# Kernel optimization log

Hardware: AMD Instinct MI355X
Metric: run time of the kernel (lower is better)

Reference implementation:

```python
import jax, jax.numpy as jnp
import numpy as np

H, W = 30, 30
D = 256
MAX_OBJECTS = 16
SENT = H * W  # sentinel label for background / invalid slots


def label_components(grid):
    """4-connected same-color connected-component labeling.
    grid: [B,H,W] int32. Returns labels [B,H,W] where each foreground cell
    carries the minimum linear index of its component (== raster-scan BFS
    discovery order of the torch code), SENT for background."""
    B = grid.shape[0]
    lin = jnp.arange(H * W, dtype=jnp.int32).reshape(1, H, W)
    fg = grid > 0
    init = jnp.where(fg, lin, SENT).astype(jnp.int32)
    big = jnp.int32(SENT)

    def nbr_min(lab):
        lp = jnp.pad(lab, ((0, 0), (1, 1), (1, 1)), constant_values=SENT)
        gp = jnp.pad(grid, ((0, 0), (1, 1), (1, 1)), constant_values=-1)
        m = lab
        for di, dj in ((-1, 0), (1, 0), (0, -1), (0, 1)):
            ls = lp[:, 1 + di:1 + di + H, 1 + dj:1 + dj + W]
            gs = gp[:, 1 + di:1 + di + H, 1 + dj:1 + dj + W]
            m = jnp.minimum(m, jnp.where(gs == grid, ls, big))
        return jnp.where(fg, m, big)

    def cond(s):
        return s[1]

    def body(s):
        lab, _ = s
        new = nbr_min(lab)
        # pointer jumping: label <- min(label, label[label]) accelerates convergence
        flat = new.reshape(B, H * W)
        jumped = jnp.take_along_axis(flat, jnp.clip(flat, 0, H * W - 1), axis=1)
        flat = jnp.where(flat < SENT, jnp.minimum(flat, jumped), SENT)
        new = flat.reshape(B, H, W)
        return new, jnp.any(new != lab)

    labels, _ = jax.lax.while_loop(cond, body, (init, jnp.array(True)))
    return labels


def extract_objects(grid, labels):
    """Per-slot (color, y, x, h, w, valid), each [B, MAX_OBJECTS]."""
    B = grid.shape[0]
    HW = H * W
    lin = jnp.arange(HW, dtype=jnp.int32)
    rows, cols = lin // W, lin % W
    lab = labels.reshape(B, HW)
    ns = HW + 1  # extra segment collects background
    seg = jnp.where(lab < SENT, lab, SENT)
    rmin = jax.vmap(lambda s: jax.ops.segment_min(rows, s, num_segments=ns))(seg)
    rmax = jax.vmap(lambda s: jax.ops.segment_max(rows, s, num_segments=ns))(seg)
    cmin = jax.vmap(lambda s: jax.ops.segment_min(cols, s, num_segments=ns))(seg)
    cmax = jax.vmap(lambda s: jax.ops.segment_max(cols, s, num_segments=ns))(seg)
    # component roots, in raster order == BFS discovery order; keep first K
    root = jnp.where((lab == lin[None, :]) & (lab < SENT), lin[None, :], SENT)
    order = jnp.sort(root, axis=1)[:, :MAX_OBJECTS]
    valid = order < SENT
    idx = jnp.clip(order, 0, HW - 1)
    bi = jnp.arange(B)[:, None]
    y = jnp.clip(rmin[bi, idx], 0, H - 1)
    x = jnp.clip(cmin[bi, idx], 0, W - 1)
    y2 = jnp.clip(rmax[bi, idx] + 1, y + 1, H)
    x2 = jnp.clip(cmax[bi, idx] + 1, x + 1, W)
    color = grid.reshape(B, HW)[bi, idx]
    return color, y, x, y2 - y, x2 - x, valid


def forward(grid_emb, structure_rep, W1, b1, W2, b2, Wp, bp, gamma, beta, ortho_scale, objs):
    color, y, x, h, w, valid = objs
    B = grid_emb.shape[0]
    bi = jnp.arange(B)[:, None]
    # summed-area table -> bbox mean-pool of grid_emb in O(1) per object
    S = jnp.pad(jnp.cumsum(jnp.cumsum(grid_emb, axis=1), axis=2),
                ((0, 0), (1, 0), (1, 0), (0, 0)))
    y2, x2 = y + h, x + w
    pool = S[bi, y2, x2] - S[bi, y, x2] - S[bi, y2, x] + S[bi, y, x]
    pool = pool / (h * w).astype(grid_emb.dtype)[..., None]       # [B,K,D]
    bbox = jnp.stack([color / 9.0, x / W, y / H, w / W, h / H], axis=-1).astype(grid_emb.dtype)
    combined = jnp.concatenate([pool, bbox], axis=-1)              # [B,K,D+5]
    hdn = jax.nn.gelu(jnp.einsum('bkf,fd->bkd', combined, W1) + b1, approximate=False)
    obj = jnp.einsum('bkd,de->bke', hdn, W2) + b2
    obj = jnp.where(valid[..., None], obj, 0.0)  # pad slots are zero embeddings
    # OrthogonalProjector with structure broadcast = mean over structure slots
    s = structure_rep.mean(axis=1, keepdims=True)                  # [B,1,D]
    sn = s / jnp.maximum(jnp.linalg.norm(s, axis=-1, keepdims=True), 1e-8)
    dot = (obj * sn).sum(axis=-1, keepdims=True)
    co = (obj - dot * sn) * ortho_scale
    co = jnp.einsum('bkd,de->bke', co, Wp) + bp
    mu = co.mean(axis=-1, keepdims=True)
    var = ((co - mu) ** 2).mean(axis=-1, keepdims=True)
    return (co - mu) / jnp.sqrt(var + 1e-5) * gamma + beta


def setup_inputs() -> dict:
    key = jax.random.key(0)
    ks = jax.random.split(key, 6)
    B, K_STRUCT = 128, 8
    grid_emb = jax.random.normal(ks[0], (B, H, W, D), dtype=jnp.float32)
    grid = jax.random.randint(ks[1], (B, H, W), 0, 10, dtype=jnp.int32)
    structure_rep = jax.random.normal(ks[2], (B, K_STRUCT, D), dtype=jnp.float32)
    sc = 0.02
    W1 = jax.random.normal(ks[3], (D + 5, D), dtype=jnp.float32) * sc
    b1 = jnp.zeros((D,), jnp.float32)
    W2 = jax.random.normal(ks[4], (D, D), dtype=jnp.float32) * sc
    b2 = jnp.zeros((D,), jnp.float32)
    Wp = jax.random.normal(ks[5], (D, D), dtype=jnp.float32) * sc
    bp = jnp.zeros((D,), jnp.float32)
    gamma = jnp.ones((D,), jnp.float32)
    beta = jnp.zeros((D,), jnp.float32)
    ortho_scale = jnp.ones((1,), jnp.float32)
    return dict(grid_emb=grid_emb, grid=grid, structure_rep=structure_rep,
                W1=W1, b1=b1, W2=W2, b2=b2, Wp=Wp, bp=bp,
                gamma=gamma, beta=beta, ortho_scale=ortho_scale)


def reference(grid_emb, grid, structure_rep, W1, b1, W2, b2, Wp, bp, gamma, beta, ortho_scale):
    labels = label_components(grid)
    objs = extract_objects(grid, labels)
    return forward(grid_emb, structure_rep, W1, b1, W2, b2, Wp, bp, gamma, beta, ortho_scale, objs)
```

## Files before the change

### kernel.cpp

```cpp
#include <hip/hip_runtime.h>
#include <math.h>

#define HH 30
#define WWID 30
#define HW 900
#define SENTV 900
#define DD 256
#define MAXK 16
#define AK 264

typedef __attribute__((ext_vector_type(8))) short short8b;
typedef __attribute__((ext_vector_type(4))) float f32x4;

__device__ __forceinline__ float gelu_exact(float x) {
    return 0.5f * x * (1.0f + erff(x * 0.70710678118654752440f));
}

__device__ __forceinline__ unsigned short f2bf(float x) {
    unsigned int u = __float_as_uint(x);
    u += 0x7FFFu + ((u >> 16) & 1u);
    return (unsigned short)(u >> 16);
}

__global__ __launch_bounds__(256) void conv_w(
    const float* __restrict__ W1, const float* __restrict__ W2,
    const float* __restrict__ Wp, unsigned short* __restrict__ ws)
{
    int f = blockIdx.x * 256 + threadIdx.x;
    int m = f >> 13;
    int rem = f & 8191;
    int ntile = rem >> 9;
    int kl = rem & 511;
    int ktile = kl >> 6;
    int lane = kl & 63;
    const float* W = (m == 0) ? W1 : (m == 1) ? W2 : Wp;
    int k0 = ktile * 32 + (lane >> 4) * 8;
    int n  = ntile * 16 + (lane & 15);
    unsigned short* dst = ws + (size_t)m * 65536 +
                          ((size_t)(ntile * 8 + ktile) * 64 + lane) * 8;
    #pragma unroll
    for (int i = 0; i < 8; ++i) dst[i] = f2bf(W[(size_t)(k0 + i) * DD + n]);
}

__device__ __forceinline__ void mfma_pass(
    const unsigned short (* __restrict__ ab)[AK],
    const unsigned short* __restrict__ wm,
    f32x4 acc[2], int cl, int tx, int wv)
{
    short8b afr[8];
    #pragma unroll
    for (int kt = 0; kt < 8; ++kt)
        afr[kt] = *(const short8b*)&ab[cl][kt * 32 + (tx >> 4) * 8];
    const short8b* base = (const short8b*)wm;
    #pragma unroll
    for (int t = 0; t < 2; ++t) {
        const int nt = wv * 2 + t;
        short8b bfr[8];
        #pragma unroll
        for (int kt = 0; kt < 8; ++kt)
            bfr[kt] = base[(nt * 8 + kt) * 64 + tx];
        #pragma unroll
        for (int kt = 0; kt < 8; ++kt)
            acc[t] = __builtin_amdgcn_mfma_f32_16x16x32_bf16(afr[kt], bfr[kt], acc[t], 0, 0, 0);
    }
}

__global__ __launch_bounds__(512, 2) void ccce_main(
    const float* __restrict__ grid_emb,
    const int* __restrict__ grid,
    const float* __restrict__ structure_rep,
    const unsigned short* __restrict__ wsw,
    const float* __restrict__ W1, const float* __restrict__ b1,
    const float* __restrict__ b2, const float* __restrict__ bp,
    const float* __restrict__ gvec, const float* __restrict__ bvec,
    const float* __restrict__ ortho_scale,
    float* __restrict__ out, int KS)
{
    const int b   = blockIdx.x >> 1;
    const int h8  = blockIdx.x & 1;
    const int tid = threadIdx.x;
    const int tx  = tid & 63;
    const int wv  = tid >> 6;
    const int cl  = tx & 15;
    const int g   = tx >> 4;

    __shared__ int color_s[HW];
    __shared__ int lab_s[HW];
    __shared__ int slot_of[HW];
    __shared__ int root_s[MAXK];
    __shared__ int nroot_s;
    __shared__ int by0[MAXK], by1[MAXK], bx0[MAXK], bx1[MAXK];
    __shared__ __align__(16) unsigned short a0[16][AK];
    __shared__ __align__(16) unsigned short a1[16][AK];
    __shared__ __align__(16) float sn_s[DD];
    __shared__ float red_s[4];
    __shared__ float feats_s[8][5];
    __shared__ float dred[8][8];
    __shared__ float lred[8][8][2];

    for (int i = tid; i < 16 * AK; i += 512) {
        ((unsigned short*)a0)[i] = 0;
        ((unsigned short*)a1)[i] = 0;
    }

    const int4* gp = (const int4*)(grid + (size_t)b * HW);
    int4 gld;
    if (tid < 225) gld = gp[tid];

    const bool do_s = (tid < DD);
    float sl0=0.f,sl1=0.f,sl2=0.f,sl3=0.f,sl4=0.f,sl5=0.f,sl6=0.f,sl7=0.f,s_gen=0.f;
    {
        const float* sr = structure_rep + (size_t)b * KS * DD + tid;
        if (do_s) {
            if (KS == 8) {
                sl0 = sr[0*DD]; sl1 = sr[1*DD]; sl2 = sr[2*DD]; sl3 = sr[3*DD];
                sl4 = sr[4*DD]; sl5 = sr[5*DD]; sl6 = sr[6*DD]; sl7 = sr[7*DD];
            } else {
                for (int j = 0; j < KS; ++j) s_gen += sr[(size_t)j * DD];
            }
        }
    }

    if (tid < 225) {
        int i = tid * 4;
        color_s[i+0] = gld.x; lab_s[i+0] = (gld.x > 0) ? (i+0) : SENTV;
        color_s[i+1] = gld.y; lab_s[i+1] = (gld.y > 0) ? (i+1) : SENTV;
        color_s[i+2] = gld.z; lab_s[i+2] = (gld.z > 0) ? (i+2) : SENTV;
        color_s[i+3] = gld.w; lab_s[i+3] = (gld.w > 0) ? (i+3) : SENTV;
    }
    __syncthreads();

    const int li0 = tid, li1 = tid + 512;
    int nm0 = 0, nm1 = 0;
    {
        int c = color_s[li0];
        if (c > 0) {
            int r = li0 / WWID, cc = li0 - (li0 / WWID) * WWID;
            nm0 = 16;
            if (r > 0       && color_s[li0 - WWID] == c) nm0 |= 1;
            if (r < HH - 1  && color_s[li0 + WWID] == c) nm0 |= 2;
            if (cc > 0      && color_s[li0 - 1]    == c) nm0 |= 4;
            if (cc < WWID-1 && color_s[li0 + 1]    == c) nm0 |= 8;
        }
    }
    if (li1 < HW) {
        int c = color_s[li1];
        if (c > 0) {
            int r = li1 / WWID, cc = li1 - (li1 / WWID) * WWID;
            nm1 = 16;
            if (r > 0       && color_s[li1 - WWID] == c) nm1 |= 1;
            if (r < HH - 1  && color_s[li1 + WWID] == c) nm1 |= 2;
            if (cc > 0      && color_s[li1 - 1]    == c) nm1 |= 4;
            if (cc < WWID-1 && color_s[li1 + 1]    == c) nm1 |= 8;
        }
    }

    for (;;) {
        int ch = 0;
        int m0 = 0, m1 = 0;
        if (nm0 & 16) {
            m0 = lab_s[li0];
            if (nm0 & 1) m0 = min(m0, lab_s[li0 - WWID]);
            if (nm0 & 2) m0 = min(m0, lab_s[li0 + WWID]);
            if (nm0 & 4) m0 = min(m0, lab_s[li0 - 1]);
            if (nm0 & 8) m0 = min(m0, lab_s[li0 + 1]);
        }
        if (nm1 & 16) {
            m1 = lab_s[li1];
            if (nm1 & 1) m1 = min(m1, lab_s[li1 - WWID]);
            if (nm1 & 2) m1 = min(m1, lab_s[li1 + WWID]);
            if (nm1 & 4) m1 = min(m1, lab_s[li1 - 1]);
            if (nm1 & 8) m1 = min(m1, lab_s[li1 + 1]);
        }
        if (nm0 & 16) m0 = min(m0, lab_s[m0]);
        if (nm1 & 16) m1 = min(m1, lab_s[m1]);
        if (nm0 & 16) m0 = min(m0, lab_s[m0]);
        if (nm1 & 16) m1 = min(m1, lab_s[m1]);
        if ((nm0 & 16) && m0 < lab_s[li0]) { lab_s[li0] = m0; ch = 1; }
        if ((nm1 & 16) && m1 < lab_s[li1]) { lab_s[li1] = m1; ch = 1; }
        if (__syncthreads_count(ch) == 0) break;
    }

    if (tid < 64) {
        int base = 0;
        for (int chk = 0; chk < 15; ++chk) {
            int cell = chk * 64 + tid;
            bool isr = (cell < HW) && (color_s[cell] > 0) && (lab_s[cell] == cell);
            unsigned long long mask = __ballot(isr);
            int rank = base + __popcll(mask & ((1ull << tid) - 1ull));
            if (isr && rank < MAXK) root_s[rank] = cell;
            base += __popcll(mask);
        }
        if (tid == 0) nroot_s = base;
    } else {
        for (int i = tid - 64; i < HW; i += 448) slot_of[i] = -1;
        if (tid >= 448 && tid < 448 + MAXK) {
            int k = tid - 448;
            by0[k] = HH; by1[k] = -1; bx0[k] = WWID; bx1[k] = -1;
        }
    }
    __syncthreads();

    const int nval = min(nroot_s, MAXK);
    if (tid < nval) slot_of[root_s[tid]] = tid;
    __syncthreads();

    if (nm0 & 16) {
        int s = slot_of[lab_s[li0]];
        if (s >= 0) {
            int r = li0 / WWID, cc = li0 - (li0 / WWID) * WWID;
            atomicMin(&by0[s], r); atomicMax(&by1[s], r);
            atomicMin(&bx0[s], cc); atomicMax(&bx1[s], cc);
        }
    }
    if (nm1 & 16) {
        int s = slot_of[lab_s[li1]];
        if (s >= 0) {
            int r = li1 / WWID, cc = li1 - (li1 / WWID) * WWID;
            atomicMin(&by0[s], r); atomicMax(&by1[s], r);
            atomicMin(&bx0[s], cc); atomicMax(&bx1[s], cc);
        }
    }

    float s_mean = (KS == 8)
        ? (sl0 + sl1 + sl2 + sl3 + sl4 + sl5 + sl6 + sl7) * 0.125f
        : s_gen * (1.0f / (float)KS);
    {
        float ss = s_mean * s_mean;
        #pragma unroll
        for (int off = 32; off > 0; off >>= 1) ss += __shfl_xor(ss, off);
        if (tx == 0 && wv < 4) red_s[wv] = ss;
    }
    __syncthreads();

    if (do_s) {
        float nrm = sqrtf(red_s[0] + red_s[1] + red_s[2] + red_s[3]);
        sn_s[tid] = s_mean / fmaxf(nrm, 1e-8f);
    }

    {
        const int slot = h8 * 8 + wv;
        const int v_ok = (slot < nval) ? 1 : 0;
        const int c0 = tx * 4;
        float4 pv = make_float4(0.f, 0.f, 0.f, 0.f);
        int y = 0, x = 0, h = 1, w = 1, col = 0;
        if (v_ok) {
            y = by0[slot]; x = bx0[slot];
            h = by1[slot] + 1 - y; w = bx1[slot] + 1 - x;
            col = color_s[root_s[slot]];
            const int n = h * w;
            const float* bp_ = grid_emb + ((size_t)(b * HH + y) * WWID + x) * DD + c0;
            float4 sum = make_float4(0.f, 0.f, 0.f, 0.f);
            for (int base2 = 0; base2 < n; base2 += 8) {
                float4 v[8];
                #pragma unroll
                for (int t = 0; t < 8; ++t) {
                    int ii = base2 + t;
                    if (ii < n) {
                        int yy = ii / w, xx = ii - yy * w;
                        v[t] = *(const float4*)(bp_ + ((size_t)yy * WWID + xx) * DD);
                    }
                }
                #pragma unroll
                for (int t = 0; t < 8; ++t) {
                    int ii = base2 + t;
                    if (ii < n) { sum.x += v[t].x; sum.y += v[t].y; sum.z += v[t].z; sum.w += v[t].w; }
                }
            }
            float inv = 1.0f / (float)n;
            pv.x = sum.x * inv; pv.y = sum.y * inv; pv.z = sum.z * inv; pv.w = sum.w * inv;
        }
        unsigned int p0 = (unsigned int)f2bf(pv.x) | ((unsigned int)f2bf(pv.y) << 16);
        unsigned int p1 = (unsigned int)f2bf(pv.z) | ((unsigned int)f2bf(pv.w) << 16);
        *(unsigned int*)&a0[wv][c0]     = p0;
        *(unsigned int*)&a0[wv][c0 + 2] = p1;
        if (tx < 5) {
            float f = 0.f;
            if (v_ok) {
                switch (tx) {
                    case 0: f = (float)col / 9.0f; break;
                    case 1: f = (float)x  / 30.0f; break;
                    case 2: f = (float)y  / 30.0f; break;
                    case 3: f = (float)w  / 30.0f; break;
                    case 4: f = (float)h  / 30.0f; break;
                }
            }
            feats_s[wv][tx] = f;
        }
    }
    __syncthreads();

    {
        f32x4 acc[2] = {{0,0,0,0},{0,0,0,0}};
        mfma_pass(a0, wsw, acc, cl, tx, wv);
        if (g < 2) {
            #pragma unroll
            for (int t = 0; t < 2; ++t) {
                int col = (wv * 2 + t) * 16 + cl;
                float b1v = b1[col];
                float tw[5];
                #pragma unroll
                for (int jj = 0; jj < 5; ++jj) tw[jj] = W1[(size_t)(256 + jj) * DD + col];
                #pragma unroll
                for (int j = 0; j < 4; ++j) {
                    int row = g * 4 + j;
                    float s = acc[t][j] + b1v;
                    #pragma unroll
                    for (int jj = 0; jj < 5; ++jj) s += feats_s[row][jj] * tw[jj];
                    a1[row][col] = f2bf(gelu_exact(s));
                }
            }
        }
        __syncthreads();
    }

    {
        f32x4 acc[2] = {{0,0,0,0},{0,0,0,0}};
        mfma_pass(a1, wsw + 65536, acc, cl, tx, wv);
        float obj[2][4], snc[2];
        if (g < 2) {
            float pd[4] = {0.f, 0.f, 0.f, 0.f};
            #pragma unroll
            for (int t = 0; t < 2; ++t) {
                int col = (wv * 2 + t) * 16 + cl;
                float b2v = b2[col];
                snc[t] = sn_s[col];
                #pragma unroll
                for (int j = 0; j < 4; ++j) {
                    int row = g * 4 + j;
                    float vm = ((h8 * 8 + row) < nval) ? 1.f : 0.f;
                    obj[t][j] = (acc[t][j] + b2v) * vm;
                    pd[j] += obj[t][j] * snc[t];
                }
            }
            #pragma unroll
            for (int off = 1; off < 16; off <<= 1) {
                #pragma unroll
                for (int j = 0; j < 4; ++j) pd[j] += __shfl_xor(pd[j], off);
            }
            if (cl == 0) {
                #pragma unroll
                for (int j = 0; j < 4; ++j) dred[wv][g * 4 + j] = pd[j];
            }
        }
        __syncthreads();
        if (g < 2) {
            float osc = ortho_scale[0];
            #pragma unroll
            for (int j = 0; j < 4; ++j) {
                int row = g * 4 + j;
                float p = 0.f;
                #pragma unroll
                for (int w = 0; w < 8; ++w) p += dred[w][row];
                #pragma unroll
                for (int t = 0; t < 2; ++t) {
                    int col = (wv * 2 + t) * 16 + cl;
                    a0[row][col] = f2bf((obj[t][j] - p * snc[t]) * osc);
                }
            }
        }
        __syncthreads();
    }

    {
        f32x4 acc[2] = {{0,0,0,0},{0,0,0,0}};
        mfma_pass(a0, wsw + 2 * 65536, acc, cl, tx, wv);
        float v[2][4];
        if (g < 2) {
            float S[4] = {0,0,0,0}, Q[4] = {0,0,0,0};
            #pragma unroll
            for (int t = 0; t < 2; ++t) {
                int col = (wv * 2 + t) * 16 + cl;
                float bpv = bp[col];
                #pragma unroll
                for (int j = 0; j < 4; ++j) {
                    v[t][j] = acc[t][j] + bpv;
                    S[j] += v[t][j];
                    Q[j] += v[t][j] * v[t][j];
                }
            }
            #pragma unroll
            for (int off = 1; off < 16; off <<= 1) {
                #pragma unroll
                for (int j = 0; j < 4; ++j) {
                    S[j] += __shfl_xor(S[j], off);
                    Q[j] += __shfl_xor(Q[j], off);
                }
            }
            if (cl == 0) {
                #pragma unroll
                for (int j = 0; j < 4; ++j) {
                    lred[wv][g * 4 + j][0] = S[j];
                    lred[wv][g * 4 + j][1] = Q[j];
                }
            }
        }
        __syncthreads();
        if (g < 2) {
            #pragma unroll
            for (int j = 0; j < 4; ++j) {
                int row = g * 4 + j;
                float Ss = 0.f, Qq = 0.f;
                #pragma unroll
                for (int w = 0; w < 8; ++w) { Ss += lred[w][row][0]; Qq += lred[w][row][1]; }
                float mu   = Ss * (1.0f / 256.0f);
                float var  = fmaxf(Qq * (1.0f / 256.0f) - mu * mu, 0.0f);
                float rstd = 1.0f / sqrtf(var + 1e-5f);
                #pragma unroll
                for (int t = 0; t < 2; ++t) {
                    int col = (wv * 2 + t) * 16 + cl;
                    float o = (v[t][j] - mu) * rstd * gvec[col] + bvec[col];
                    out[((size_t)(b * MAXK + h8 * 8 + row)) * DD + col] = o;
                }
            }
        }
    }
}

extern "C" void kernel_launch(void* const* d_in, const int* in_sizes, int n_in,
                              void* d_out, int out_size, void* d_ws, size_t ws_size,
                              hipStream_t stream) {
    const float* grid_emb = (const float*)d_in[0];
    const int*   grid     = (const int*)d_in[1];
    const float* srep     = (const float*)d_in[2];
    const float* W1v = (const float*)d_in[3];
    const float* b1v = (const float*)d_in[4];
    const float* W2v = (const float*)d_in[5];
    const float* b2v = (const float*)d_in[6];
    const float* Wpv = (const float*)d_in[7];
    const float* bpv = (const float*)d_in[8];
    const float* gv  = (const float*)d_in[9];
    const float* bv  = (const float*)d_in[10];
    const float* osv = (const float*)d_in[11];
    float* out = (float*)d_out;

    const int B  = in_sizes[1] / HW;
    const int KS = in_sizes[2] / (B * DD);

    unsigned short* wsw = (unsigned short*)d_ws;
    hipLaunchKernelGGL(conv_w, dim3(96), dim3(256), 0, stream,
                       W1v, W2v, Wpv, wsw);
    hipLaunchKernelGGL(ccce_main, dim3(B * 2), dim3(512), 0, stream,
                       grid_emb, grid, srep, wsw, W1v, b1v, b2v, bpv,
                       gv, bv, osv, out, KS);
}
```

Measured before the change: 28.85 us.

## Use one 1024-thread block per batch instead of two half-blocks

Each batch element now runs in a single 1024-thread block, where before two 512-thread blocks each redundantly labeled the components and handled 8 of the 16 object slots. Every thread owns one grid cell, and each of the 16 waves computes one 16-column tile of all 16 rows through the MFMA layers, so all four MFMA row groups hold real data. The labeling loop now does an extra synchronized relaxation sweep per iteration, and the zero-fill of the activation buffers is removed. This halves the block count and removes the duplicated labeling work, at the cost of fewer blocks in flight and more waves per barrier.

Result: faster. 27.81 us (-3.6%).

```diff
diff --git a/kernel.cpp b/kernel.cpp
--- a/kernel.cpp
+++ b/kernel.cpp
@@ -42,30 +42,26 @@
     for (int i = 0; i < 8; ++i) dst[i] = f2bf(W[(size_t)(k0 + i) * DD + n]);
 }
 
-__device__ __forceinline__ void mfma_pass(
+__device__ __forceinline__ void mfma_pass16(
     const unsigned short (* __restrict__ ab)[AK],
     const unsigned short* __restrict__ wm,
-    f32x4 acc[2], int cl, int tx, int wv)
+    f32x4* acc, int cl, int tx, int wv)
 {
     short8b afr[8];
     #pragma unroll
     for (int kt = 0; kt < 8; ++kt)
         afr[kt] = *(const short8b*)&ab[cl][kt * 32 + (tx >> 4) * 8];
     const short8b* base = (const short8b*)wm;
+    short8b bfr[8];
     #pragma unroll
-    for (int t = 0; t < 2; ++t) {
-        const int nt = wv * 2 + t;
-        short8b bfr[8];
-        #pragma unroll
-        for (int kt = 0; kt < 8; ++kt)
-            bfr[kt] = base[(nt * 8 + kt) * 64 + tx];
-        #pragma unroll
-        for (int kt = 0; kt < 8; ++kt)
-            acc[t] = __builtin_amdgcn_mfma_f32_16x16x32_bf16(afr[kt], bfr[kt], acc[t], 0, 0, 0);
-    }
-}
-
-__global__ __launch_bounds__(512, 2) void ccce_main(
+    for (int kt = 0; kt < 8; ++kt)
+        bfr[kt] = base[(wv * 8 + kt) * 64 + tx];
+    #pragma unroll
+    for (int kt = 0; kt < 8; ++kt)
+        *acc = __builtin_amdgcn_mfma_f32_16x16x32_bf16(afr[kt], bfr[kt], *acc, 0, 0, 0);
+}
+
+__global__ __launch_bounds__(1024, 4) void ccce_main(
     const float* __restrict__ grid_emb,
     const int* __restrict__ grid,
     const float* __restrict__ structure_rep,
@@ -76,8 +72,7 @@
     const float* __restrict__ ortho_scale,
     float* __restrict__ out, int KS)
 {
-    const int b   = blockIdx.x >> 1;
-    const int h8  = blockIdx.x & 1;
+    const int b   = blockIdx.x;
     const int tid = threadIdx.x;
     const int tx  = tid & 63;
     const int wv  = tid >> 6;
@@ -94,14 +89,9 @@
     __shared__ __align__(16) unsigned short a1[16][AK];
     __shared__ __align__(16) float sn_s[DD];
     __shared__ float red_s[4];
-    __shared__ float feats_s[8][5];
-    __shared__ float dred[8][8];
-    __shared__ float lred[8][8][2];
-
-    for (int i = tid; i < 16 * AK; i += 512) {
-        ((unsigned short*)a0)[i] = 0;
-        ((unsigned short*)a1)[i] = 0;
-    }
+    __shared__ float feats_s[16][5];
+    __shared__ float dred[16][16];
+    __shared__ float lred[16][16][2];
 
     const int4* gp = (const int4*)(grid + (size_t)b * HW);
     int4 gld;
@@ -130,54 +120,43 @@
     }
     __syncthreads();
 
-    const int li0 = tid, li1 = tid + 512;
-    int nm0 = 0, nm1 = 0;
-    {
-        int c = color_s[li0];
+    const int li = tid;
+    int nm = 0;
+    if (li < HW) {
+        int c = color_s[li];
         if (c > 0) {
-            int r = li0 / WWID, cc = li0 - (li0 / WWID) * WWID;
-            nm0 = 16;
-            if (r > 0       && color_s[li0 - WWID] == c) nm0 |= 1;
-            if (r < HH - 1  && color_s[li0 + WWID] == c) nm0 |= 2;
-            if (cc > 0      && color_s[li0 - 1]    == c) nm0 |= 4;
-            if (cc < WWID-1 && color_s[li0 + 1]    == c) nm0 |= 8;
-        }
-    }
-    if (li1 < HW) {
-        int c = color_s[li1];
-        if (c > 0) {
-            int r = li1 / WWID, cc = li1 - (li1 / WWID) * WWID;
-            nm1 = 16;
-            if (r > 0       && color_s[li1 - WWID] == c) nm1 |= 1;
-            if (r < HH - 1  && color_s[li1 + WWID] == c) nm1 |= 2;
-            if (cc > 0      && color_s[li1 - 1]    == c) nm1 |= 4;
-            if (cc < WWID-1 && color_s[li1 + 1]    == c) nm1 |= 8;
+            int r = li / WWID, cc = li - (li / WWID) * WWID;
+            nm = 16;
+            if (r > 0       && color_s[li - WWID] == c) nm |= 1;
+            if (r < HH - 1  && color_s[li + WWID] == c) nm |= 2;
+            if (cc > 0      && color_s[li - 1]    == c) nm |= 4;
+            if (cc < WWID-1 && color_s[li + 1]    == c) nm |= 8;
         }
     }
 
     for (;;) {
+        if (nm & 16) {
+            int m = lab_s[li];
+            if (nm & 1) m = min(m, lab_s[li - WWID]);
+            if (nm & 2) m = min(m, lab_s[li + WWID]);
+            if (nm & 4) m = min(m, lab_s[li - 1]);
+            if (nm & 8) m = min(m, lab_s[li + 1]);
+            m = min(m, lab_s[m]);
+            m = min(m, lab_s[m]);
+            if (m < lab_s[li]) lab_s[li] = m;
+        }
+        __syncthreads();
         int ch = 0;
-        int m0 = 0, m1 = 0;
-        if (nm0 & 16) {
-            m0 = lab_s[li0];
-            if (nm0 & 1) m0 = min(m0, lab_s[li0 - WWID]);
-            if (nm0 & 2) m0 = min(m0, lab_s[li0 + WWID]);
-            if (nm0 & 4) m0 = min(m0, lab_s[li0 - 1]);
-            if (nm0 & 8) m0 = min(m0, lab_s[li0 + 1]);
-        }
-        if (nm1 & 16) {
-            m1 = lab_s[li1];
-            if (nm1 & 1) m1 = min(m1, lab_s[li1 - WWID]);
-            if (nm1 & 2) m1 = min(m1, lab_s[li1 + WWID]);
-            if (nm1 & 4) m1 = min(m1, lab_s[li1 - 1]);
-            if (nm1 & 8) m1 = min(m1, lab_s[li1 + 1]);
-        }
-        if (nm0 & 16) m0 = min(m0, lab_s[m0]);
-        if (nm1 & 16) m1 = min(m1, lab_s[m1]);
-        if (nm0 & 16) m0 = min(m0, lab_s[m0]);
-        if (nm1 & 16) m1 = min(m1, lab_s[m1]);
-        if ((nm0 & 16) && m0 < lab_s[li0]) { lab_s[li0] = m0; ch = 1; }
-        if ((nm1 & 16) && m1 < lab_s[li1]) { lab_s[li1] = m1; ch = 1; }
+        if (nm & 16) {
+            int m = lab_s[li];
+            if (nm & 1) m = min(m, lab_s[li - WWID]);
+            if (nm & 2) m = min(m, lab_s[li + WWID]);
+            if (nm & 4) m = min(m, lab_s[li - 1]);
+            if (nm & 8) m = min(m, lab_s[li + 1]);
+            m = min(m, lab_s[m]);
+            m = min(m, lab_s[m]);
+            if (m < lab_s[li]) { lab_s[li] = m; ch = 1; }
+        }
         if (__syncthreads_count(ch) == 0) break;
     }
 
@@ -193,9 +172,9 @@
         }
         if (tid == 0) nroot_s = base;
     } else {
-        for (int i = tid - 64; i < HW; i += 448) slot_of[i] = -1;
-        if (tid >= 448 && tid < 448 + MAXK) {
-            int k = tid - 448;
+        for (int i = tid - 64; i < HW; i += 960) slot_of[i] = -1;
+        if (tid >= 960 && tid < 960 + MAXK) {
+            int k = tid - 960;
             by0[k] = HH; by1[k] = -1; bx0[k] = WWID; bx1[k] = -1;
         }
     }
@@ -205,18 +184,10 @@
     if (tid < nval) slot_of[root_s[tid]] = tid;
     __syncthreads();
 
-    if (nm0 & 16) {
-        int s = slot_of[lab_s[li0]];
+    if (nm & 16) {
+        int s = slot_of[lab_s[li]];
         if (s >= 0) {
-            int r = li0 / WWID, cc = li0 - (li0 / WWID) * WWID;
-            atomicMin(&by0[s], r); atomicMax(&by1[s], r);
-            atomicMin(&bx0[s], cc); atomicMax(&bx1[s], cc);
-        }
-    }
-    if (nm1 & 16) {
-        int s = slot_of[lab_s[li1]];
-        if (s >= 0) {
-            int r = li1 / WWID, cc = li1 - (li1 / WWID) * WWID;
+            int r = li / WWID, cc = li - (li / WWID) * WWID;
             atomicMin(&by0[s], r); atomicMax(&by1[s], r);
             atomicMin(&bx0[s], cc); atomicMax(&bx1[s], cc);
         }
@@ -239,7 +210,7 @@
     }
 
     {
-        const int slot = h8 * 8 + wv;
+        const int slot = wv;
         const int v_ok = (slot < nval) ? 1 : 0;
         const int c0 = tx * 4;
         float4 pv = make_float4(0.f, 0.f, 0.f, 0.f);
@@ -291,128 +262,100 @@
     __syncthreads();
 
     {
-        f32x4 acc[2] = {{0,0,0,0},{0,0,0,0}};
-        mfma_pass(a0, wsw, acc, cl, tx, wv);
-        if (g < 2) {
-            #pragma unroll
-            for (int t = 0; t < 2; ++t) {
-                int col = (wv * 2 + t) * 16 + cl;
-                float b1v = b1[col];
-                float tw[5];
-                #pragma unroll
-                for (int jj = 0; jj < 5; ++jj) tw[jj] = W1[(size_t)(256 + jj) * DD + col];
-                #pragma unroll
-                for (int j = 0; j < 4; ++j) {
-                    int row = g * 4 + j;
-                    float s = acc[t][j] + b1v;
-                    #pragma unroll
-                    for (int jj = 0; jj < 5; ++jj) s += feats_s[row][jj] * tw[jj];
-                    a1[row][col] = f2bf(gelu_exact(s));
-                }
-            }
-        }
-        __syncthreads();
-    }
-
-    {
-        f32x4 acc[2] = {{0,0,0,0},{0,0,0,0}};
-        mfma_pass(a1, wsw + 65536, acc, cl, tx, wv);
-        float obj[2][4], snc[2];
-        if (g < 2) {
-            float pd[4] = {0.f, 0.f, 0.f, 0.f};
-            #pragma unroll
-            for (int t = 0; t < 2; ++t) {
-                int col = (wv * 2 + t) * 16 + cl;
-                float b2v = b2[col];
-                snc[t] = sn_s[col];
-                #pragma unroll
-                for (int j = 0; j < 4; ++j) {
-                    int row = g * 4 + j;
-                    float vm = ((h8 * 8 + row) < nval) ? 1.f : 0.f;
-                    obj[t][j] = (acc[t][j] + b2v) * vm;
-                    pd[j] += obj[t][j] * snc[t];
-                }
-            }
-            #pragma unroll
-            for (int off = 1; off < 16; off <<= 1) {
-                #pragma unroll
-                for (int j = 0; j < 4; ++j) pd[j] += __shfl_xor(pd[j], off);
-            }
-            if (cl == 0) {
-                #pragma unroll
-                for (int j = 0; j < 4; ++j) dred[wv][g * 4 + j] = pd[j];
-            }
-        }
-        __syncthreads();
-        if (g < 2) {
-            float osc = ortho_scale[0];
+        f32x4 acc = {0, 0, 0, 0};
+        mfma_pass16(a0, wsw, &acc, cl, tx, wv);
+        const int col = wv * 16 + cl;
+        float b1v = b1[col];
+        float tw[5];
+        #pragma unroll
+        for (int jj = 0; jj < 5; ++jj) tw[jj] = W1[(size_t)(256 + jj) * DD + col];
+        #pragma unroll
+        for (int j = 0; j < 4; ++j) {
+            int row = g * 4 + j;
+            float s = acc[j] + b1v;
+            #pragma unroll
+            for (int jj = 0; jj < 5; ++jj) s += feats_s[row][jj] * tw[jj];
+            a1[row][col] = f2bf(gelu_exact(s));
+        }
+        __syncthreads();
+    }
+
+    {
+        f32x4 acc = {0, 0, 0, 0};
+        mfma_pass16(a1, wsw + 65536, &acc, cl, tx, wv);
+        const int col = wv * 16 + cl;
+        float b2v = b2[col];
+        float snc = sn_s[col];
+        float obj[4];
+        float pd[4];
+        #pragma unroll
+        for (int j = 0; j < 4; ++j) {
+            int row = g * 4 + j;
+            float vm = (row < nval) ? 1.f : 0.f;
+            obj[j] = (acc[j] + b2v) * vm;
+            pd[j] = obj[j] * snc;
+        }
+        #pragma unroll
+        for (int off = 1; off < 16; off <<= 1) {
+            #pragma unroll
+            for (int j = 0; j < 4; ++j) pd[j] += __shfl_xor(pd[j], off);
+        }
+        if (cl == 0) {
+            #pragma unroll
+            for (int j = 0; j < 4; ++j) dred[wv][g * 4 + j] = pd[j];
+        }
+        __syncthreads();
+        float osc = ortho_scale[0];
+        #pragma unroll
+        for (int j = 0; j < 4; ++j) {
+            int row = g * 4 + j;
+            float p = 0.f;
+            #pragma unroll
+            for (int w = 0; w < 16; ++w) p += dred[w][row];
+            a0[row][col] = f2bf((obj[j] - p * snc) * osc);
+        }
+        __syncthreads();
+    }
+
+    {
+        f32x4 acc = {0, 0, 0, 0};
+        mfma_pass16(a0, wsw + 2 * 65536, &acc, cl, tx, wv);
+        const int col = wv * 16 + cl;
+        float bpv = bp[col];
+        float v[4], S[4], Q[4];
+        #pragma unroll
+        for (int j = 0; j < 4; ++j) {
+            v[j] = acc[j] + bpv;
+            S[j] = v[j];
+            Q[j] = v[j] * v[j];
+        }
+        #pragma unroll
+        for (int off = 1; off < 16; off <<= 1) {
             #pragma unroll
             for (int j = 0; j < 4; ++j) {
-                int row = g * 4 + j;
-                float p = 0.f;
-                #pragma unroll
-                for (int w = 0; w < 8; ++w) p += dred[w][row];
-                #pragma unroll
-                for (int t = 0; t < 2; ++t) {
-                    int col = (wv * 2 + t) * 16 + cl;
-                    a0[row][col] = f2bf((obj[t][j] - p * snc[t]) * osc);
-                }
-            }
-        }
-        __syncthreads();
-    }
-
-    {
-        f32x4 acc[2] = {{0,0,0,0},{0,0,0,0}};
-        mfma_pass(a0, wsw + 2 * 65536, acc, cl, tx, wv);
-        float v[2][4];
-        if (g < 2) {
-            float S[4] = {0,0,0,0}, Q[4] = {0,0,0,0};
-            #pragma unroll
-            for (int t = 0; t < 2; ++t) {
-                int col = (wv * 2 + t) * 16 + cl;
-                float bpv = bp[col];
-                #pragma unroll
-                for (int j = 0; j < 4; ++j) {
-                    v[t][j] = acc[t][j] + bpv;
-                    S[j] += v[t][j];
-                    Q[j] += v[t][j] * v[t][j];
-                }
-            }
-            #pragma unroll
-            for (int off = 1; off < 16; off <<= 1) {
-                #pragma unroll
-                for (int j = 0; j < 4; ++j) {
-                    S[j] += __shfl_xor(S[j], off);
-                    Q[j] += __shfl_xor(Q[j], off);
-                }
-            }
-            if (cl == 0) {
-                #pragma unroll
-                for (int j = 0; j < 4; ++j) {
-                    lred[wv][g * 4 + j][0] = S[j];
-                    lred[wv][g * 4 + j][1] = Q[j];
-                }
-            }
-        }
-        __syncthreads();
-        if (g < 2) {
+                S[j] += __shfl_xor(S[j], off);
+                Q[j] += __shfl_xor(Q[j], off);
+            }
+        }
+        if (cl == 0) {
             #pragma unroll
             for (int j = 0; j < 4; ++j) {
-                int row = g * 4 + j;
-                float Ss = 0.f, Qq = 0.f;
-                #pragma unroll
-                for (int w = 0; w < 8; ++w) { Ss += lred[w][row][0]; Qq += lred[w][row][1]; }
-                float mu   = Ss * (1.0f / 256.0f);
-                float var  = fmaxf(Qq * (1.0f / 256.0f) - mu * mu, 0.0f);
-                float rstd = 1.0f / sqrtf(var + 1e-5f);
-                #pragma unroll
-                for (int t = 0; t < 2; ++t) {
-                    int col = (wv * 2 + t) * 16 + cl;
-                    float o = (v[t][j] - mu) * rstd * gvec[col] + bvec[col];
-                    out[((size_t)(b * MAXK + h8 * 8 + row)) * DD + col] = o;
-                }
-            }
+                lred[wv][g * 4 + j][0] = S[j];
+                lred[wv][g * 4 + j][1] = Q[j];
+            }
+        }
+        __syncthreads();
+        float gvc = gvec[col], bvc = bvec[col];
+        #pragma unroll
+        for (int j = 0; j < 4; ++j) {
+            int row = g * 4 + j;
+            float Ss = 0.f, Qq = 0.f;
+            #pragma unroll
+            for (int w = 0; w < 16; ++w) { Ss += lred[w][row][0]; Qq += lred[w][row][1]; }
+            float mu   = Ss * (1.0f / 256.0f);
+            float var  = fmaxf(Qq * (1.0f / 256.0f) - mu * mu, 0.0f);
+            float rstd = 1.0f / sqrtf(var + 1e-5f);
+            out[((size_t)(b * MAXK + row)) * DD + col] = (v[j] - mu) * rstd * gvc + bvc;
         }
     }
 }
@@ -440,7 +383,7 @@
     unsigned short* wsw = (unsigned short*)d_ws;
     hipLaunchKernelGGL(conv_w, dim3(96), dim3(256), 0, stream,
                        W1v, W2v, Wpv, wsw);
-    hipLaunchKernelGGL(ccce_main, dim3(B * 2), dim3(512), 0, stream,
+    hipLaunchKernelGGL(ccce_main, dim3(B), dim3(1024), 0, stream,
                        grid_emb, grid, srep, wsw, W1v, b1v, b2v, bpv,
                        gv, bv, osv, out, KS);
 }
```
